# Performance work log

Measured on AMD Instinct MI355X. Metric: run time of the kernel, lower is better.

The kernel has to match this reference:

```python
import jax, jax.numpy as jnp
import numpy as np

IN_CH = 256
OUT_CH = 256
STATE = 384
OUT_SEQ = 32
B_SZ = 8
SEQ = 512


def setup_inputs() -> dict:
    key = jax.random.key(0)
    ks = jax.random.split(key, 8)
    rmin, rmax, max_phase = 0.0, 1.0, 6.283
    u1 = jax.random.uniform(ks[0], (STATE,))
    u2 = jax.random.uniform(ks[1], (STATE,))
    # standard LRU stable-ring initialization
    nu_log = jnp.log(-0.5 * jnp.log(u1 * (rmax + rmin) * (rmax - rmin) + rmin ** 2))
    theta_log = jnp.log(max_phase * u2)
    lam_mod = jnp.exp(-jnp.exp(nu_log))
    gamma_log = jnp.log(jnp.sqrt(1.0 - lam_mod ** 2))
    B_re = jax.random.normal(ks[2], (STATE, IN_CH)) / np.sqrt(2 * IN_CH)
    B_im = jax.random.normal(ks[3], (STATE, IN_CH)) / np.sqrt(2 * IN_CH)
    C_re = jax.random.normal(ks[4], (OUT_CH, STATE)) / np.sqrt(STATE)
    C_im = jax.random.normal(ks[5], (OUT_CH, STATE)) / np.sqrt(STATE)
    D = jax.random.normal(ks[6], (OUT_CH, IN_CH)) / np.sqrt(IN_CH)
    x = jax.random.normal(ks[7], (B_SZ, SEQ, IN_CH))
    return dict(x=x, nu_log=nu_log, theta_log=theta_log, gamma_log=gamma_log,
                B_re=B_re, B_im=B_im, C_re=C_re, C_im=C_im, D=D)


def _lru(x, h_re, h_im, nu_log, theta_log, gamma_log, B_re, B_im, C_re, C_im, D):
    """One LRU pass over a full sequence. x: [B,S,C]. h_*: [B,N] initial complex state.
    Diagonal complex recurrence h_t = Lambda*h_{t-1} + gamma*(B x_t); y_t = Re(C h_t) + D x_t."""
    lam_mod = jnp.exp(-jnp.exp(nu_log))              # |Lambda| in (0,1)
    lre = lam_mod * jnp.cos(jnp.exp(theta_log))      # [N]
    lim = lam_mod * jnp.sin(jnp.exp(theta_log))
    gamma = jnp.exp(gamma_log)
    # input projection for whole sequence (complex, split into re/im)
    u_re = gamma * jnp.einsum('bsc,nc->bsn', x, B_re)  # [B,S,N]
    u_im = gamma * jnp.einsum('bsc,nc->bsn', x, B_im)

    def step(h, u):
        hre, him = h
        ur, ui = u
        nre = lre * hre - lim * him + ur
        nim = lre * him + lim * hre + ui
        return (nre, nim), (nre, nim)

    (h_re, h_im), (hs_re, hs_im) = jax.lax.scan(
        step, (h_re, h_im),
        (jnp.swapaxes(u_re, 0, 1), jnp.swapaxes(u_im, 0, 1)))  # scan over S
    hs_re = jnp.swapaxes(hs_re, 0, 1)  # [B,S,N]
    hs_im = jnp.swapaxes(hs_im, 0, 1)
    y = (jnp.einsum('bsn,on->bso', hs_re, C_re)
         - jnp.einsum('bsn,on->bso', hs_im, C_im)
         + jnp.einsum('bsc,oc->bso', x, D))
    return y, h_re, h_im


def reference(x, nu_log, theta_log, gamma_log, B_re, B_im, C_re, C_im, D):
    bsz = x.shape[0]
    h_re = jnp.zeros((bsz, STATE), x.dtype)   # state=None on first call -> zeros
    h_im = jnp.zeros((bsz, STATE), x.dtype)
    outs = []
    for _ in range(OUT_SEQ):
        x, h_re, h_im = _lru(x, h_re, h_im, nu_log, theta_log, gamma_log,
                             B_re, B_im, C_re, C_im, D)
        outs.append(x[:, -1:])
    return jnp.concatenate(outs, axis=-2)  # [B, OUT_SEQ, OUT_CH]
```

## Files before the change

kernel.cpp:

```cpp
#include <hip/hip_runtime.h>
#include <hip/hip_bf16.h>
#include <math.h>

typedef unsigned short u16;
typedef __attribute__((ext_vector_type(8))) short bf16x8;
typedef __attribute__((ext_vector_type(4))) float f32x4;

#define IN_CH   256
#define STATE   384
#define OUT_SEQ 32
#define B_SZ    8
#define SEQ     512
#define M_ROWS  4096
#define NJ      768

#define PS_WB  (NJ*IN_CH)
#define PS_WC  (IN_CH*NJ)
#define PS_WD  (IN_CH*IN_CH)
#define PS_Z   ((size_t)M_ROWS*NJ)
#define PS_X   ((size_t)M_ROWS*IN_CH)

static constexpr size_t B_U   = 0;
static constexpr size_t B_Z   = B_U  + 8*(size_t)M_ROWS*IN_CH*4;
static constexpr size_t B_XA  = B_Z  + 3*(size_t)M_ROWS*NJ*2;
static constexpr size_t B_XB  = B_XA + 3*(size_t)M_ROWS*IN_CH*2;
static constexpr size_t B_WB  = B_XB + 3*(size_t)M_ROWS*IN_CH*2;
static constexpr size_t B_WC  = B_WB + 3*(size_t)PS_WB*2;
static constexpr size_t B_WD  = B_WC + 3*(size_t)PS_WC*2;
static constexpr size_t B_LAM = B_WD + 3*(size_t)PS_WD*2;
static constexpr size_t B_HC  = B_LAM + 2*768*4;

__device__ __forceinline__ u16 f2b(float v) {
    __hip_bfloat16 h = __float2bfloat16(v);
    return *(u16*)&h;
}
__device__ __forceinline__ float b2f(u16 u) {
    __hip_bfloat16 h = *(__hip_bfloat16*)&u;
    return __bfloat162float(h);
}
__device__ __forceinline__ void split3(float v, u16& a, u16& b, u16& c) {
    a = f2b(v);  float r1 = v  - b2f(a);
    b = f2b(r1); float r2 = r1 - b2f(b);
    c = f2b(r2);
}

__device__ __forceinline__ size_t a_idx(int row, int k, int NKC) {
    return ((size_t)(((row >> 5)*NKC + (k >> 5))*2 + ((k >> 4) & 1))*2 + ((k >> 3) & 1))*256
           + (size_t)(row & 31)*8 + (k & 7);
}

__device__ __forceinline__ void frag_decode(int r, int& t32, int& h, int& hi5,
                                            int& lo5, int& e) {
    t32 = r >> 10; int r2 = r & 1023;
    h = r2 >> 9;   int r3 = r2 & 511;
    hi5 = r3 >> 8; int r4 = r3 & 255;
    lo5 = r4 >> 3; e = r4 & 7;
}

__global__ void prep_lam_hc(const float* __restrict__ nu_log,
                            const float* __restrict__ th_log,
                            float* __restrict__ lam, float* __restrict__ lam32,
                            float* __restrict__ hc0) {
    int n = threadIdx.x;
    if (n < STATE) {
        float lm = expf(-expf(nu_log[n]));
        float th = expf(th_log[n]);
        float ar = lm * cosf(th), ai = lm * sinf(th);
        lam[2*n] = ar; lam[2*n+1] = ai;
        float pr = ar, pi = ai;
#pragma unroll
        for (int i = 0; i < 5; ++i) {
            float nr = pr*pr - pi*pi, ni = 2.f*pr*pi;
            pr = nr; pi = ni;
        }
        lam32[2*n] = pr; lam32[2*n+1] = pi;
    }
    for (int i = threadIdx.x; i < B_SZ*NJ; i += blockDim.x) hc0[i] = 0.f;
}

__global__ void prep_wb(const float* __restrict__ B_re, const float* __restrict__ B_im,
                        const float* __restrict__ gamma_log, u16* __restrict__ W) {
    int idx = blockIdx.x*blockDim.x + threadIdx.x;
    int c32 = idx >> 13, r = idx & 8191;
    int t32,h,hi5,lo5,e; frag_decode(r, t32,h,hi5,lo5,e);
    int j = c32*32 + lo5;
    int k = t32*32 + (2*h + hi5)*8 + e;
    int n = j >> 1;
    float g = expf(gamma_log[n]);
    float v = g * ((j & 1) ? B_im[n*IN_CH + k] : B_re[n*IN_CH + k]);
    u16 a,b,cc; split3(v,a,b,cc);
    W[idx] = a; W[idx + PS_WB] = b; W[idx + 2*PS_WB] = cc;
}

__global__ void prep_wcd(const float* __restrict__ C_re, const float* __restrict__ C_im,
                         const float* __restrict__ D,
                         u16* __restrict__ WC, u16* __restrict__ WD) {
    int idx = blockIdx.x*blockDim.x + threadIdx.x;
    if (idx < PS_WC) {
        int c32 = idx / 24576, r = idx % 24576;
        int t32,h,hi5,lo5,e; frag_decode(r, t32,h,hi5,lo5,e);
        int o = c32*32 + lo5;
        int j = t32*32 + (2*h + hi5)*8 + e;
        int n = j >> 1;
        float v = (j & 1) ? -C_im[o*STATE + n] : C_re[o*STATE + n];
        u16 a,b,c; split3(v,a,b,c);
        WC[idx] = a; WC[idx + PS_WC] = b; WC[idx + 2*PS_WC] = c;
    } else {
        int q = idx - PS_WC;
        int c32 = q >> 13, r = q & 8191;
        int t32,h,hi5,lo5,e; frag_decode(r, t32,h,hi5,lo5,e);
        int o = c32*32 + lo5;
        int c = t32*32 + (2*h + hi5)*8 + e;
        float v = D[o*IN_CH + c];
        u16 a,b,cc; split3(v,a,b,cc);
        WD[q] = a; WD[q + PS_WD] = b; WD[q + 2*PS_WD] = cc;
    }
}

__global__ void prep_x(const float* __restrict__ x,
                       u16* __restrict__ X1, u16* __restrict__ X2, u16* __restrict__ X3) {
    int idx = blockIdx.x*blockDim.x + threadIdx.x;
    int row = idx >> 8, k = idx & 255;
    u16 a,b,c; split3(x[idx],a,b,c);
    size_t o = a_idx(row, k, 8);
    X1[o] = a; X2[o] = b; X3[o] = c;
}

__device__ __constant__ const int cPI[6] = {0,0,1,0,1,2};
__device__ __constant__ const int cPJ[6] = {0,1,0,2,1,0};

struct G1P { const u16* A[3]; };

__global__ __launch_bounds__(512, 4)
void front_k(G1P ga, const u16* __restrict__ WBp,
             u16* __restrict__ Z1, u16* __restrict__ Z2, u16* __restrict__ Z3,
             const float* __restrict__ lam, const float* __restrict__ lam32,
             const float2* __restrict__ HcIn, float2* __restrict__ HcOut) {
    __shared__ __align__(16) float Ls[512*33];
    __shared__ float2 car[32][16];
    __shared__ float2 hp[32][16];
    const int tid = threadIdx.x, lane = tid & 63, w = tid >> 6;
    const int b = blockIdx.x, jt = blockIdx.y;
    const int l15 = lane & 15, q = lane >> 4;
    const int hb = q >> 1, hi5q = q & 1;

    f32x4 acc[4][2];
#pragma unroll
    for (int i = 0; i < 4; ++i)
#pragma unroll
        for (int n16 = 0; n16 < 2; ++n16) acc[i][n16] = 0.f;

#pragma unroll
    for (int kc = 0; kc < 8; ++kc) {
        bf16x8 av[4][3], bv[2][3];
#pragma unroll
        for (int p = 0; p < 3; ++p) {
#pragma unroll
            for (int i = 0; i < 4; ++i) {
                int m16 = i*8 + w;
                int row32 = b*16 + (m16 >> 1);
                int rin = ((m16 & 1) << 4) + l15;
                av[i][p] = *(const bf16x8*)(ga.A[p]
                    + ((((size_t)(row32*8 + kc)*2 + hb)*2 + hi5q) << 8) + rin*8);
            }
#pragma unroll
            for (int n16 = 0; n16 < 2; ++n16)
                bv[n16][p] = *(const bf16x8*)(WBp + (size_t)p*PS_WB
                    + ((((size_t)(jt*8 + kc)*2 + hb)*2 + hi5q) << 8) + (n16*16 + l15)*8);
        }
#pragma unroll
        for (int t6 = 0; t6 < 6; ++t6)
#pragma unroll
            for (int i = 0; i < 4; ++i)
#pragma unroll
                for (int n16 = 0; n16 < 2; ++n16)
                    acc[i][n16] = __builtin_amdgcn_mfma_f32_16x16x32_bf16(
                        av[i][cPI[t6]], bv[n16][cPJ[t6]], acc[i][n16], 0, 0, 0);
    }

#pragma unroll
    for (int i = 0; i < 4; ++i) {
        int m16 = i*8 + w;
#pragma unroll
        for (int n16 = 0; n16 < 2; ++n16)
#pragma unroll
            for (int r = 0; r < 4; ++r) {
                int s = m16*16 + q*4 + r;
                int jl = n16*16 + l15;
                Ls[s*33 + jl] = acc[i][n16][r];
            }
    }
    __syncthreads();

    if (tid < 256) {
        int st = tid & 15, ch = tid >> 4;
        int n = jt*16 + st;
        float lre = lam[2*n], lim = lam[2*n+1];
        float hr = 0.f, hm = 0.f;
        for (int t = 0; t < 32; ++t) {
            int s = ch*32 + t;
            float ur = Ls[s*33 + 2*st], ui = Ls[s*33 + 2*st + 1];
            float nr = fmaf(lre, hr, fmaf(-lim, hm, ur));
            float nm = fmaf(lre, hm, fmaf( lim, hr, ui));
            hr = nr; hm = nm;
        }
        car[ch][st] = make_float2(hr, hm);
    }
    __syncthreads();

    if (tid < 16) {
        int st = tid, n = jt*16 + st;
        float l32r = lam32[2*n], l32i = lam32[2*n+1];
        float2 hh = HcIn[(size_t)b*STATE + n];
        hp[0][st] = hh;
        for (int ch = 1; ch < 16; ++ch) {
            float2 cj = car[ch-1][st];
            float nr = fmaf(l32r, hh.x, fmaf(-l32i, hh.y, cj.x));
            float ni = fmaf(l32r, hh.y, fmaf( l32i, hh.x, cj.y));
            hh.x = nr; hh.y = ni;
            hp[ch][st] = hh;
        }
    }
    __syncthreads();

    if (tid < 256) {
        int st = tid & 15, ch = tid >> 4;
        int n = jt*16 + st;
        float lre = lam[2*n], lim = lam[2*n+1];
        float2 hh = hp[ch][st];
        int j0 = jt*32 + 2*st;
        for (int t = 0; t < 32; ++t) {
            int s = ch*32 + t;
            float ur = Ls[s*33 + 2*st], ui = Ls[s*33 + 2*st + 1];
            float nr = fmaf(lre, hh.x, fmaf(-lim, hh.y, ur));
            float ni = fmaf(lre, hh.y, fmaf( lim, hh.x, ui));
            hh.x = nr; hh.y = ni;
            u16 a1,a2,a3, c1,c2,c3;
            split3(nr, a1,a2,a3);
            split3(ni, c1,c2,c3);
            size_t zo = a_idx(b*512 + s, j0, 24);
            ushort2 t2;
            t2.x = a1; t2.y = c1; *(ushort2*)(Z1 + zo) = t2;
            t2.x = a2; t2.y = c2; *(ushort2*)(Z2 + zo) = t2;
            t2.x = a3; t2.y = c3; *(ushort2*)(Z3 + zo) = t2;
        }
        if (ch == 15) HcOut[(size_t)b*STATE + n] = hh;
    }
}

struct G2P {
    const u16* Z[3]; const u16* X[3]; const u16* WC; const u16* WD;
    u16* O1; u16* O2; u16* O3; float* outp; int iter;
};

__global__ __launch_bounds__(512, 2)
void gemm2_k(G2P g) {
    __shared__ __align__(16) float Lred[64*64];
    const int tid = threadIdx.x, lane = tid & 63, w = tid >> 6;
    const int kg = w >> 2, wq = w & 3;
    const int wr = wq & 1, wcq = wq >> 1;
    const int m0 = blockIdx.x*64, n0 = blockIdx.y*64;
    const int hi5 = lane >> 5, lo5 = lane & 31;
    const int c32 = (n0 >> 5) + wcq;
    const int m32 = blockIdx.x*2 + wr;
    const int cbase = kg*16;

    f32x4 acc4[4];
    float acc[16];
#pragma unroll
    for (int i = 0; i < 16; ++i) acc[i] = 0.f;
    typedef __attribute__((ext_vector_type(16))) float f32x16_t;
    f32x16_t accv;
#pragma unroll
    for (int i = 0; i < 16; ++i) accv[i] = 0.f;
    (void)acc4; (void)acc;

    auto aptr = [&](int p, int c, int h) -> const u16* {
        if (c < 24)
            return g.Z[p] + ((((size_t)(m32*24 + c)*2 + h)*2 + hi5) << 8) + lo5*8;
        return g.X[p] + ((((size_t)(m32*8 + (c - 24))*2 + h)*2 + hi5) << 8) + lo5*8;
    };
    auto bptr = [&](int p, int c, int h) -> const u16* {
        if (c < 24)
            return g.WC + (size_t)p*PS_WC
                   + ((((size_t)(c32*24 + c)*2 + h)*2 + hi5) << 8) + lo5*8;
        return g.WD + (size_t)p*PS_WD
               + ((((size_t)(c32*8 + (c - 24))*2 + h)*2 + hi5) << 8) + lo5*8;
    };

    bf16x8 bwin[3][4][2];
    auto loadB = [&](int wnd, int tlo, int thi) {
#pragma unroll
        for (int p = 0; p < 3; ++p)
#pragma unroll
            for (int t = 0; t < 4; ++t) {
                if (t < tlo || t >= thi) continue;
#pragma unroll
                for (int h = 0; h < 2; ++h)
                    bwin[p][t][h] = *(const bf16x8*)bptr(p, cbase + wnd*4 + t, h);
            }
    };
    bf16x8 av[2][3][2];
    auto loadA = [&](int buf, int t) {
#pragma unroll
        for (int p = 0; p < 3; ++p)
#pragma unroll
            for (int h = 0; h < 2; ++h)
                av[buf][p][h] = *(const bf16x8*)aptr(p, cbase + t, h);
    };

    loadA(0, 0);
    loadB(0, 0, 4);
    loadA(1, 1);
#pragma unroll
    for (int t = 0; t < 16; ++t) {
        if ((t & 3) == 2 && t < 12) loadB((t >> 2) + 1, 0, 2);
        const int cb = t & 1;
        const int tw = t & 3;
#pragma unroll
        for (int t6 = 0; t6 < 6; ++t6)
            accv = __builtin_amdgcn_mfma_f32_32x32x16_bf16(
                av[cb][cPI[t6]][0], bwin[cPJ[t6]][tw][0],
                __builtin_amdgcn_mfma_f32_32x32x16_bf16(
                    av[cb][cPI[t6]][1], bwin[cPJ[t6]][tw][1], accv, 0, 0, 0),
                0, 0, 0);
        if ((t & 3) == 3 && t < 12) loadB((t >> 2) + 1, 2, 4);
        if (t + 2 < 16) loadA(cb, t + 2);
    }

    if (kg == 1) {
#pragma unroll
        for (int reg = 0; reg < 16; ++reg) {
            int rl = wr*32 + (reg & 3) + 8*(reg >> 2) + 4*hi5;
            int cl = wcq*32 + lo5;
            Lred[rl*64 + cl] = accv[reg];
        }
    }
    __syncthreads();
    if (kg == 0) {
#pragma unroll
        for (int reg = 0; reg < 16; ++reg) {
            int rl = wr*32 + (reg & 3) + 8*(reg >> 2) + 4*hi5;
            int cl = wcq*32 + lo5;
            float v = accv[reg] + Lred[rl*64 + cl];
            int row = m0 + rl, col = n0 + cl;
            u16 a,b,c; split3(v, a,b,c);
            size_t o = a_idx(row, col, 8);
            g.O1[o] = a; g.O2[o] = b; g.O3[o] = c;
            if ((row & (SEQ-1)) == SEQ-1)
                g.outp[(size_t)((row >> 9)*OUT_SEQ + g.iter)*IN_CH + col] = v;
        }
    }
}

extern "C" void kernel_launch(void* const* d_in, const int* in_sizes, int n_in,
                              void* d_out, int out_size, void* d_ws, size_t ws_size,
                              hipStream_t stream) {
    const float* x_in      = (const float*)d_in[0];
    const float* nu_log    = (const float*)d_in[1];
    const float* theta_log = (const float*)d_in[2];
    const float* gamma_log = (const float*)d_in[3];
    const float* B_re      = (const float*)d_in[4];
    const float* B_im      = (const float*)d_in[5];
    const float* C_re      = (const float*)d_in[6];
    const float* C_im      = (const float*)d_in[7];
    const float* D         = (const float*)d_in[8];
    float* out = (float*)d_out;

    char* ws = (char*)d_ws;
    u16* Z1 = (u16*)(ws + B_Z);
    u16* Z2 = Z1 + PS_Z;
    u16* Z3 = Z2 + PS_Z;
    u16* XA1 = (u16*)(ws + B_XA);
    u16* XA2 = XA1 + PS_X;
    u16* XA3 = XA2 + PS_X;
    u16* XB1 = (u16*)(ws + B_XB);
    u16* XB2 = XB1 + PS_X;
    u16* XB3 = XB2 + PS_X;
    u16* WB  = (u16*)(ws + B_WB);
    u16* WCt = (u16*)(ws + B_WC);
    u16* WDt = (u16*)(ws + B_WD);
    float* lam   = (float*)(ws + B_LAM);
    float* lam32 = lam + 768;
    float2* Hc0  = (float2*)(ws + B_HC);
    float2* Hc1  = Hc0 + (size_t)B_SZ*STATE;

    prep_lam_hc<<<1, 384, 0, stream>>>(nu_log, theta_log, lam, lam32, (float*)Hc0);
    prep_wb<<<PS_WB/256, 256, 0, stream>>>(B_re, B_im, gamma_log, WB);
    prep_wcd<<<(PS_WC + PS_WD)/256, 256, 0, stream>>>(C_re, C_im, D, WCt, WDt);
    prep_x<<<(M_ROWS*IN_CH)/256, 256, 0, stream>>>(x_in, XA1, XA2, XA3);

    for (int it = 0; it < OUT_SEQ; ++it) {
        u16* Xc[3]; u16* Xn[3];
        if (it & 1) { Xc[0]=XB1; Xc[1]=XB2; Xc[2]=XB3; Xn[0]=XA1; Xn[1]=XA2; Xn[2]=XA3; }
        else        { Xc[0]=XA1; Xc[1]=XA2; Xc[2]=XA3; Xn[0]=XB1; Xn[1]=XB2; Xn[2]=XB3; }
        float2* Hin  = (it & 1) ? Hc1 : Hc0;
        float2* Hout = (it & 1) ? Hc0 : Hc1;

        G1P g1;
        for (int p = 0; p < 3; ++p) g1.A[p] = Xc[p];
        front_k<<<dim3(B_SZ, 24), 512, 0, stream>>>(
            g1, WB, Z1, Z2, Z3, lam, lam32, Hin, Hout);

        G2P g2;
        g2.Z[0]=Z1; g2.Z[1]=Z2; g2.Z[2]=Z3;
        g2.X[0]=Xc[0]; g2.X[1]=Xc[1]; g2.X[2]=Xc[2];
        g2.WC = WCt; g2.WD = WDt;
        g2.O1 = Xn[0]; g2.O2 = Xn[1]; g2.O3 = Xn[2];
        g2.outp = out; g2.iter = it;
        gemm2_k<<<dim3(M_ROWS/64, IN_CH/64), 512, 0, stream>>>(g2);
    }
}
```

Before: 1.332 ms.

## Double-buffer front GEMM loads and split scan into 32 chunks across all threads

The front kernel now double-buffers its A/B register fragments so the loads for chunk kc+2 are issued during the MFMAs on chunk kc. The chunked scan uses all 512 threads with 32 chunks of 16 steps instead of 256 threads with 16 chunks of 32, so the carry combine uses lambda^16 over 31 steps. The LDS row stride moves from 33 to 34 so u can be read as float2. The grid is flattened to 1D with batch in the low bits and launch bounds relaxed to 2 waves, trading occupancy and registers for latency hiding and more scan parallelism.

Result: no change. 1.330 ms (-0.2%).

```diff
diff --git a/kernel.cpp b/kernel.cpp
--- a/kernel.cpp
+++ b/kernel.cpp
@@ -59,7 +59,7 @@
 
 __global__ void prep_lam_hc(const float* __restrict__ nu_log,
                             const float* __restrict__ th_log,
-                            float* __restrict__ lam, float* __restrict__ lam32,
+                            float* __restrict__ lam, float* __restrict__ lam16,
                             float* __restrict__ hc0) {
     int n = threadIdx.x;
     if (n < STATE) {
@@ -69,11 +69,11 @@
         lam[2*n] = ar; lam[2*n+1] = ai;
         float pr = ar, pi = ai;
 #pragma unroll
-        for (int i = 0; i < 5; ++i) {
+        for (int i = 0; i < 4; ++i) {
             float nr = pr*pr - pi*pi, ni = 2.f*pr*pi;
             pr = nr; pi = ni;
         }
-        lam32[2*n] = pr; lam32[2*n+1] = pi;
+        lam16[2*n] = pr; lam16[2*n+1] = pi;
     }
     for (int i = threadIdx.x; i < B_SZ*NJ; i += blockDim.x) hc0[i] = 0.f;
 }
@@ -131,16 +131,16 @@
 
 struct G1P { const u16* A[3]; };
 
-__global__ __launch_bounds__(512, 4)
+__global__ __launch_bounds__(512, 2)
 void front_k(G1P ga, const u16* __restrict__ WBp,
              u16* __restrict__ Z1, u16* __restrict__ Z2, u16* __restrict__ Z3,
-             const float* __restrict__ lam, const float* __restrict__ lam32,
+             const float* __restrict__ lam, const float* __restrict__ lam16,
              const float2* __restrict__ HcIn, float2* __restrict__ HcOut) {
-    __shared__ __align__(16) float Ls[512*33];
+    __shared__ __align__(16) float Ls[512*34];
     __shared__ float2 car[32][16];
     __shared__ float2 hp[32][16];
     const int tid = threadIdx.x, lane = tid & 63, w = tid >> 6;
-    const int b = blockIdx.x, jt = blockIdx.y;
+    const int b = blockIdx.x & 7, jt = blockIdx.x >> 3;
     const int l15 = lane & 15, q = lane >> 4;
     const int hb = q >> 1, hi5q = q & 1;
 
@@ -150,24 +150,33 @@
 #pragma unroll
         for (int n16 = 0; n16 < 2; ++n16) acc[i][n16] = 0.f;
 
-#pragma unroll
-    for (int kc = 0; kc < 8; ++kc) {
-        bf16x8 av[4][3], bv[2][3];
-#pragma unroll
-        for (int p = 0; p < 3; ++p) {
+    bf16x8 av[2][4][3], bv[2][2][3];
+    auto loadA = [&](int buf, int kc) {
+#pragma unroll
+        for (int p = 0; p < 3; ++p)
 #pragma unroll
             for (int i = 0; i < 4; ++i) {
                 int m16 = i*8 + w;
                 int row32 = b*16 + (m16 >> 1);
                 int rin = ((m16 & 1) << 4) + l15;
-                av[i][p] = *(const bf16x8*)(ga.A[p]
+                av[buf][i][p] = *(const bf16x8*)(ga.A[p]
                     + ((((size_t)(row32*8 + kc)*2 + hb)*2 + hi5q) << 8) + rin*8);
             }
+    };
+    auto loadB = [&](int buf, int kc) {
+#pragma unroll
+        for (int p = 0; p < 3; ++p)
 #pragma unroll
             for (int n16 = 0; n16 < 2; ++n16)
-                bv[n16][p] = *(const bf16x8*)(WBp + (size_t)p*PS_WB
+                bv[buf][n16][p] = *(const bf16x8*)(WBp + (size_t)p*PS_WB
                     + ((((size_t)(jt*8 + kc)*2 + hb)*2 + hi5q) << 8) + (n16*16 + l15)*8);
-        }
+    };
+
+    loadA(0, 0); loadB(0, 0);
+    loadA(1, 1); loadB(1, 1);
+#pragma unroll
+    for (int kc = 0; kc < 8; ++kc) {
+        const int cb = kc & 1;
 #pragma unroll
         for (int t6 = 0; t6 < 6; ++t6)
 #pragma unroll
@@ -175,7 +184,8 @@
 #pragma unroll
                 for (int n16 = 0; n16 < 2; ++n16)
                     acc[i][n16] = __builtin_amdgcn_mfma_f32_16x16x32_bf16(
-                        av[i][cPI[t6]], bv[n16][cPJ[t6]], acc[i][n16], 0, 0, 0);
+                        av[cb][i][cPI[t6]], bv[cb][n16][cPJ[t6]], acc[i][n16], 0, 0, 0);
+        if (kc + 2 < 8) { loadA(cb, kc + 2); loadB(cb, kc + 2); }
     }
 
 #pragma unroll
@@ -187,21 +197,22 @@
             for (int r = 0; r < 4; ++r) {
                 int s = m16*16 + q*4 + r;
                 int jl = n16*16 + l15;
-                Ls[s*33 + jl] = acc[i][n16][r];
+                Ls[s*34 + jl] = acc[i][n16][r];
             }
     }
     __syncthreads();
 
-    if (tid < 256) {
+    {
         int st = tid & 15, ch = tid >> 4;
         int n = jt*16 + st;
         float lre = lam[2*n], lim = lam[2*n+1];
         float hr = 0.f, hm = 0.f;
-        for (int t = 0; t < 32; ++t) {
-            int s = ch*32 + t;
-            float ur = Ls[s*33 + 2*st], ui = Ls[s*33 + 2*st + 1];
-            float nr = fmaf(lre, hr, fmaf(-lim, hm, ur));
-            float nm = fmaf(lre, hm, fmaf( lim, hr, ui));
+#pragma unroll
+        for (int t = 0; t < 16; ++t) {
+            int s = ch*16 + t;
+            float2 u = *(const float2*)&Ls[s*34 + 2*st];
+            float nr = fmaf(lre, hr, fmaf(-lim, hm, u.x));
+            float nm = fmaf(lre, hm, fmaf( lim, hr, u.y));
             hr = nr; hm = nm;
         }
         car[ch][st] = make_float2(hr, hm);
@@ -210,30 +221,32 @@
 
     if (tid < 16) {
         int st = tid, n = jt*16 + st;
-        float l32r = lam32[2*n], l32i = lam32[2*n+1];
+        float l16r = lam16[2*n], l16i = lam16[2*n+1];
         float2 hh = HcIn[(size_t)b*STATE + n];
         hp[0][st] = hh;
-        for (int ch = 1; ch < 16; ++ch) {
+#pragma unroll
+        for (int ch = 1; ch < 32; ++ch) {
             float2 cj = car[ch-1][st];
-            float nr = fmaf(l32r, hh.x, fmaf(-l32i, hh.y, cj.x));
-            float ni = fmaf(l32r, hh.y, fmaf( l32i, hh.x, cj.y));
+            float nr = fmaf(l16r, hh.x, fmaf(-l16i, hh.y, cj.x));
+            float ni = fmaf(l16r, hh.y, fmaf( l16i, hh.x, cj.y));
             hh.x = nr; hh.y = ni;
             hp[ch][st] = hh;
         }
     }
     __syncthreads();
 
-    if (tid < 256) {
+    {
         int st = tid & 15, ch = tid >> 4;
         int n = jt*16 + st;
         float lre = lam[2*n], lim = lam[2*n+1];
         float2 hh = hp[ch][st];
         int j0 = jt*32 + 2*st;
-        for (int t = 0; t < 32; ++t) {
-            int s = ch*32 + t;
-            float ur = Ls[s*33 + 2*st], ui = Ls[s*33 + 2*st + 1];
-            float nr = fmaf(lre, hh.x, fmaf(-lim, hh.y, ur));
-            float ni = fmaf(lre, hh.y, fmaf( lim, hh.x, ui));
+#pragma unroll
+        for (int t = 0; t < 16; ++t) {
+            int s = ch*16 + t;
+            float2 u = *(const float2*)&Ls[s*34 + 2*st];
+            float nr = fmaf(lre, hh.x, fmaf(-lim, hh.y, u.x));
+            float ni = fmaf(lre, hh.y, fmaf( lim, hh.x, u.y));
             hh.x = nr; hh.y = ni;
             u16 a1,a2,a3, c1,c2,c3;
             split3(nr, a1,a2,a3);
@@ -244,7 +257,7 @@
             t2.x = a2; t2.y = c2; *(ushort2*)(Z2 + zo) = t2;
             t2.x = a3; t2.y = c3; *(ushort2*)(Z3 + zo) = t2;
         }
-        if (ch == 15) HcOut[(size_t)b*STATE + n] = hh;
+        if (ch == 31) HcOut[(size_t)b*STATE + n] = hh;
     }
 }
 
@@ -265,15 +278,10 @@
     const int m32 = blockIdx.x*2 + wr;
     const int cbase = kg*16;
 
-    f32x4 acc4[4];
-    float acc[16];
-#pragma unroll
-    for (int i = 0; i < 16; ++i) acc[i] = 0.f;
     typedef __attribute__((ext_vector_type(16))) float f32x16_t;
     f32x16_t accv;
 #pragma unroll
     for (int i = 0; i < 16; ++i) accv[i] = 0.f;
-    (void)acc4; (void)acc;
 
     auto aptr = [&](int p, int c, int h) -> const u16* {
         if (c < 24)
@@ -381,11 +389,11 @@
     u16* WCt = (u16*)(ws + B_WC);
     u16* WDt = (u16*)(ws + B_WD);
     float* lam   = (float*)(ws + B_LAM);
-    float* lam32 = lam + 768;
+    float* lam16 = lam + 768;
     float2* Hc0  = (float2*)(ws + B_HC);
     float2* Hc1  = Hc0 + (size_t)B_SZ*STATE;
 
-    prep_lam_hc<<<1, 384, 0, stream>>>(nu_log, theta_log, lam, lam32, (float*)Hc0);
+    prep_lam_hc<<<1, 384, 0, stream>>>(nu_log, theta_log, lam, lam16, (float*)Hc0);
     prep_wb<<<PS_WB/256, 256, 0, stream>>>(B_re, B_im, gamma_log, WB);
     prep_wcd<<<(PS_WC + PS_WD)/256, 256, 0, stream>>>(C_re, C_im, D, WCt, WDt);
     prep_x<<<(M_ROWS*IN_CH)/256, 256, 0, stream>>>(x_in, XA1, XA2, XA3);
@@ -399,8 +407,8 @@
 
         G1P g1;
         for (int p = 0; p < 3; ++p) g1.A[p] = Xc[p];
-        front_k<<<dim3(B_SZ, 24), 512, 0, stream>>>(
-            g1, WB, Z1, Z2, Z3, lam, lam32, Hin, Hout);
+        front_k<<<192, 512, 0, stream>>>(
+            g1, WB, Z1, Z2, Z3, lam, lam16, Hin, Hout);
 
         G2P g2;
         g2.Z[0]=Z1; g2.Z[1]=Z2; g2.Z[2]=Z3;
```
